# Performance work log

Hardware: AMD Instinct MI355X
Metric: run time of the kernel (lower is better)

Reference implementation:

```python
import jax, jax.numpy as jnp
import numpy as np

N, D, NUM_CLASSES = 4096, 512, 128
MARGIN = 0.3


def setup_inputs() -> dict:
    key = jax.random.key(0)
    k1, k2 = jax.random.split(key)
    embeddings = jax.random.normal(k1, (N, D), dtype=jnp.float32)
    labels = jax.random.randint(k2, (N,), 0, NUM_CLASSES, dtype=jnp.int64)
    return {"embeddings": embeddings, "labels": labels}


def _batch_hard_triplet(embeddings, labels, margin):
    # L2-normalize rows (torch F.normalize: x / max(||x||, eps))
    norm = jnp.linalg.norm(embeddings, axis=1, keepdims=True)
    e = embeddings / jnp.maximum(norm, 1e-12)
    n = e.shape[0]
    # Pairwise Euclidean distance via Gram matrix; ||a-b||^2 = 2 - 2 a.b for unit vectors
    gram = e @ e.T                                   # [N, N]
    sq = jnp.clip(2.0 - 2.0 * gram, 0.0, None)
    # safe sqrt: zero (and exactly-equal) pairs get distance 0 with zero gradient
    nz = sq > 0
    dist = jnp.where(nz, jnp.sqrt(jnp.where(nz, sq, 1.0)), 0.0)  # [N, N]

    same = labels[:, None] == labels[None, :]        # [N, N] bool
    eye = jnp.eye(n, dtype=bool)
    pos_mask = same & ~eye                           # positives excluding self
    neg_mask = ~same

    # hardest positive (row max over positives), hardest negative (row min over negatives)
    dist_ap = jnp.max(jnp.where(pos_mask, dist, -jnp.inf), axis=1)  # [N]
    dist_an = jnp.min(jnp.where(neg_mask, dist, jnp.inf), axis=1)   # [N]

    valid = jnp.any(pos_mask, axis=1) & jnp.any(neg_mask, axis=1)   # rows kept by torch loop
    per_row = jax.nn.relu(dist_ap - dist_an + margin)
    num_valid = jnp.sum(valid)
    loss_sum = jnp.sum(jnp.where(valid, per_row, 0.0))
    return jnp.where(num_valid > 0, loss_sum / jnp.maximum(num_valid, 1), 0.0)


def reference(embeddings, labels):
    return _batch_hard_triplet(embeddings, labels, MARGIN)
```

## Files before the change

### kernel.cpp

```cpp
#include <hip/hip_runtime.h>
#include <hip/hip_bf16.h>
#include <stdint.h>


#define NROW 4096
#define DIM  512
#define MARGIN 0.3f
#define BT 128
#define NTILE (NROW / BT)
#define NPAIR (NTILE * (NTILE + 1) / 2)
#define NBLK  (NPAIR * 2)
#define POS_INIT 0xFFFFFFFFu
#define NEG_INIT 0u

typedef __attribute__((ext_vector_type(8))) __bf16 bf16x8;
typedef __attribute__((ext_vector_type(4))) float  f32x4;
typedef __attribute__((ext_vector_type(8))) unsigned short u16x8;

__device__ __forceinline__ unsigned enc(float f) {
    unsigned u = __float_as_uint(f);
    return (u & 0x80000000u) ? ~u : (u | 0x80000000u);
}
__device__ __forceinline__ float dec(unsigned e) {
    return (e & 0x80000000u) ? __uint_as_float(e & 0x7fffffffu)
                             : __uint_as_float(~e);
}

__device__ __forceinline__ unsigned short f2bf(float f) {
    __hip_bfloat16 h = __float2bfloat16(f);
    return *reinterpret_cast<unsigned short*>(&h);
}

__global__ void tl_norm(const float* __restrict__ E,
                        __hip_bfloat16* __restrict__ Ebf,
                        unsigned* __restrict__ posArr,
                        unsigned* __restrict__ negArr) {
    if (blockIdx.x < 16) {
        int t = blockIdx.x * 256 + threadIdx.x;
        posArr[t] = POS_INIT;
        negArr[t] = NEG_INIT;
    }
    const int wave  = threadIdx.x >> 6;
    const int lane  = threadIdx.x & 63;
    const int r2    = lane >> 4;
    const int kc    = lane & 15;
    const int rtile = blockIdx.x;
    const int r_in  = wave * 4 + r2;
    const int row   = rtile * 16 + r_in;

    const float4* src = (const float4*)(E + (size_t)row * DIM) + kc * 8;
    float4 v[8];
    #pragma unroll
    for (int i = 0; i < 8; i++) v[i] = src[i];

    float ss = 0.0f;
    #pragma unroll
    for (int i = 0; i < 8; i++)
        ss += v[i].x*v[i].x + v[i].y*v[i].y + v[i].z*v[i].z + v[i].w*v[i].w;
    #pragma unroll
    for (int m = 1; m < 16; m <<= 1) ss += __shfl_xor(ss, m);
    const float inv = 1.0f / fmaxf(sqrtf(ss), 1e-12f);

    u16x8* dst = (u16x8*)Ebf + (size_t)kc * 16384 + (size_t)rtile * 64 + r_in;
    #pragma unroll
    for (int c = 0; c < 4; c++) {
        const float4 lo = v[2*c], hi = v[2*c + 1];
        u16x8 o;
        o[0] = f2bf(lo.x * inv); o[1] = f2bf(lo.y * inv);
        o[2] = f2bf(lo.z * inv); o[3] = f2bf(lo.w * inv);
        o[4] = f2bf(hi.x * inv); o[5] = f2bf(hi.y * inv);
        o[6] = f2bf(hi.z * inv); o[7] = f2bf(hi.w * inv);
        dst[c * 16] = o;
    }
}

__global__ void __launch_bounds__(256, 3)
tl_gram(const __hip_bfloat16* __restrict__ Ebf,
        const int* __restrict__ labels,
        unsigned* __restrict__ posArr,
        unsigned* __restrict__ negArr) {
    __shared__ int rowLab[BT];
    __shared__ int colLab[64];

    const int bid = blockIdx.x;
    const int swz = (bid & 7) * (NBLK / 8) + (bid >> 3);
    int t = swz >> 1;
    const int h = swz & 1;

    int bi = 0, rowlen = NTILE;
    while (t >= rowlen) { t -= rowlen; rowlen--; bi++; }
    const int bj = bi + t;

    const int tid  = threadIdx.x;
    const int wave = tid >> 6;
    const int lane = tid & 63;
    const int quad = lane >> 4;
    const int l16  = lane & 15;
    const int wr   = wave >> 1;
    const int wc   = wave & 1;
    const int tileI = bi * BT;
    const int tileJ = bj * BT + h * 64;
    const bool diag = (bi == bj);

    if (tid < BT)            rowLab[tid] = labels[tileI + tid];
    else if (tid < BT + 64)  colLab[tid - BT] = labels[tileJ + (tid - BT)];
    __syncthreads();

    const bf16x8* Ev = (const bf16x8*)Ebf;
    const bf16x8* Ea = Ev + ((tileI + wr * 64) >> 4) * 64 + lane;
    const bf16x8* Eb = Ev + ((tileJ + wc * 32) >> 4) * 64 + lane;

    f32x4 acc[4][2] = {};
    bf16x8 a[4][4], b[4][2];

    #pragma unroll
    for (int p = 0; p < 3; ++p) {
        #pragma unroll
        for (int mi = 0; mi < 4; mi++) a[p][mi] = Ea[p * 16384 + mi * 64];
        #pragma unroll
        for (int ni = 0; ni < 2; ni++) b[p][ni] = Eb[p * 16384 + ni * 64];
    }
    #pragma unroll
    for (int kk = 0; kk < 16; ++kk) {
        const int cur = kk & 3;
        if (kk + 3 < 16) {
            const int nx = (kk + 3) & 3;
            #pragma unroll
            for (int mi = 0; mi < 4; mi++)
                a[nx][mi] = Ea[(kk + 3) * 16384 + mi * 64];
            #pragma unroll
            for (int ni = 0; ni < 2; ni++)
                b[nx][ni] = Eb[(kk + 3) * 16384 + ni * 64];
        }
        #pragma unroll
        for (int mi = 0; mi < 4; mi++)
            #pragma unroll
            for (int ni = 0; ni < 2; ni++)
                acc[mi][ni] = __builtin_amdgcn_mfma_f32_16x16x32_bf16(
                    a[cur][mi], b[cur][ni], acc[mi][ni], 0, 0, 0);
    }

    int rl[16], cl[2], clocv[2];
    #pragma unroll
    for (int mi = 0; mi < 4; mi++)
        #pragma unroll
        for (int reg = 0; reg < 4; reg++)
            rl[mi * 4 + reg] = rowLab[wr * 64 + mi * 16 + quad * 4 + reg];
    #pragma unroll
    for (int ni = 0; ni < 2; ni++) {
        clocv[ni] = wc * 32 + ni * 16 + l16;
        cl[ni] = colLab[clocv[ni]];
    }

    #pragma unroll
    for (int mi = 0; mi < 4; mi++) {
        #pragma unroll
        for (int reg = 0; reg < 4; reg++) {
            const int rloc = wr * 64 + mi * 16 + quad * 4 + reg;
            const int lr   = rl[mi * 4 + reg];
            const int gi   = tileI + rloc;
            float pmin =  INFINITY;
            float nmax = -INFINITY;
            #pragma unroll
            for (int ni = 0; ni < 2; ni++) {
                const int gj  = tileJ + clocv[ni];
                const float g = acc[mi][ni][reg];
                const bool same = (lr == cl[ni]);
                if (same && gi != gj) pmin = fminf(pmin, g);
                if (!same)            nmax = fmaxf(nmax, g);
            }
            #pragma unroll
            for (int m = 1; m < 16; m <<= 1) {
                pmin = fminf(pmin, __shfl_xor(pmin, m));
                nmax = fmaxf(nmax, __shfl_xor(nmax, m));
            }
            if (l16 == 0) {
                if (pmin <  INFINITY) atomicMin(&posArr[gi], enc(pmin));
                if (nmax > -INFINITY) atomicMax(&negArr[gi], enc(nmax));
            }
        }
    }

    if (!diag) {
        #pragma unroll
        for (int ni = 0; ni < 2; ni++) {
            const int lc = cl[ni];
            const int gj = tileJ + clocv[ni];
            float pmin =  INFINITY;
            float nmax = -INFINITY;
            #pragma unroll
            for (int mi = 0; mi < 4; mi++) {
                #pragma unroll
                for (int reg = 0; reg < 4; reg++) {
                    const float g = acc[mi][ni][reg];
                    const bool same = (rl[mi * 4 + reg] == lc);
                    if (same) pmin = fminf(pmin, g);
                    else      nmax = fmaxf(nmax, g);
                }
            }
            pmin = fminf(pmin, __shfl_xor(pmin, 16));
            pmin = fminf(pmin, __shfl_xor(pmin, 32));
            nmax = fmaxf(nmax, __shfl_xor(nmax, 16));
            nmax = fmaxf(nmax, __shfl_xor(nmax, 32));
            if (quad == 0) {
                if (pmin <  INFINITY) atomicMin(&posArr[gj], enc(pmin));
                if (nmax > -INFINITY) atomicMax(&negArr[gj], enc(nmax));
            }
        }
    }
}

__global__ void tl_final(const unsigned* __restrict__ posArr,
                         const unsigned* __restrict__ negArr,
                         float* __restrict__ out) {
    const int tid = threadIdx.x;
    uint4 pe4 = ((const uint4*)posArr)[tid];
    uint4 ne4 = ((const uint4*)negArr)[tid];
    unsigned pes[4] = {pe4.x, pe4.y, pe4.z, pe4.w};
    unsigned nes[4] = {ne4.x, ne4.y, ne4.z, ne4.w};
    float sum = 0.0f;
    int   count = 0;
    #pragma unroll
    for (int j = 0; j < 4; j++) {
        const bool valid = (pes[j] != POS_INIT) && (nes[j] != NEG_INIT);
        const float dap = sqrtf(fmaxf(2.0f - 2.0f * dec(pes[j]), 0.0f));
        const float dan = sqrtf(fmaxf(2.0f - 2.0f * dec(nes[j]), 0.0f));
        const float per = fmaxf(dap - dan + MARGIN, 0.0f);
        if (valid) { sum += per; count += 1; }
    }
    #pragma unroll
    for (int m = 32; m >= 1; m >>= 1) {
        sum   += __shfl_xor(sum, m);
        count += __shfl_xor(count, m);
    }
    __shared__ float ssum[16];
    __shared__ int   scnt[16];
    const int wave = tid >> 6, lane = tid & 63;
    if (lane == 0) { ssum[wave] = sum; scnt[wave] = count; }
    __syncthreads();
    if (tid == 0) {
        float s = 0.0f; int c = 0;
        #pragma unroll
        for (int w = 0; w < 16; w++) { s += ssum[w]; c += scnt[w]; }
        out[0] = (c > 0) ? (s / (float)c) : 0.0f;
    }
}

extern "C" void kernel_launch(void* const* d_in, const int* in_sizes, int n_in,
                              void* d_out, int out_size, void* d_ws, size_t ws_size,
                              hipStream_t stream) {
    const float* E      = (const float*)d_in[0];
    const int*   labels = (const int*)d_in[1];
    float*       out    = (float*)d_out;

    char* ws = (char*)d_ws;
    __hip_bfloat16* Ebf   = (__hip_bfloat16*)ws;
    unsigned* posArr      = (unsigned*)(ws + (size_t)NROW * DIM * 2);
    unsigned* negArr      = posArr + NROW;

    tl_norm<<<NROW / 16, 256, 0, stream>>>(E, Ebf, posArr, negArr);
    tl_gram<<<NBLK, 256, 0, stream>>>(Ebf, labels, posArr, negArr);
    tl_final<<<1, 1024, 0, stream>>>(posArr, negArr, out);
}
```

Before: 101.9 us.

## Use full 128x128 Gram tiles per block instead of split 128x64 halves

Each block now computes a full 128x128 tile pair, so each wave computes a 64x64 sub-tile with 4x4 MFMA accumulators instead of 64x32. This halves the block count and raises operand reuse per loaded fragment, cutting global/L2 loads of B operands and duplicate row-side atomics. Occupancy drops (launch bounds 3→2) because register pressure increases, and sched_barriers are added to pin load/MFMA ordering. Only 528 blocks remain for 256 CUs, so wave quantization and load imbalance may get worse.

Result: faster. 92.60 us (-9.1%).

```diff
diff --git a/kernel.cpp b/kernel.cpp
--- a/kernel.cpp
+++ b/kernel.cpp
@@ -9,7 +9,6 @@
 #define BT 128
 #define NTILE (NROW / BT)
 #define NPAIR (NTILE * (NTILE + 1) / 2)
-#define NBLK  (NPAIR * 2)
 #define POS_INIT 0xFFFFFFFFu
 #define NEG_INIT 0u
 
@@ -74,18 +73,16 @@
     }
 }
 
-__global__ void __launch_bounds__(256, 3)
+__global__ void __launch_bounds__(256, 2)
 tl_gram(const __hip_bfloat16* __restrict__ Ebf,
         const int* __restrict__ labels,
         unsigned* __restrict__ posArr,
         unsigned* __restrict__ negArr) {
     __shared__ int rowLab[BT];
-    __shared__ int colLab[64];
+    __shared__ int colLab[BT];
 
     const int bid = blockIdx.x;
-    const int swz = (bid & 7) * (NBLK / 8) + (bid >> 3);
-    int t = swz >> 1;
-    const int h = swz & 1;
+    int t = (bid & 7) * (NPAIR / 8) + (bid >> 3);
 
     int bi = 0, rowlen = NTILE;
     while (t >= rowlen) { t -= rowlen; rowlen--; bi++; }
@@ -99,56 +96,60 @@
     const int wr   = wave >> 1;
     const int wc   = wave & 1;
     const int tileI = bi * BT;
-    const int tileJ = bj * BT + h * 64;
+    const int tileJ = bj * BT;
     const bool diag = (bi == bj);
 
-    if (tid < BT)            rowLab[tid] = labels[tileI + tid];
-    else if (tid < BT + 64)  colLab[tid - BT] = labels[tileJ + (tid - BT)];
+    if (tid < BT) rowLab[tid] = labels[tileI + tid];
+    else          colLab[tid - BT] = labels[tileJ + (tid - BT)];
     __syncthreads();
 
     const bf16x8* Ev = (const bf16x8*)Ebf;
     const bf16x8* Ea = Ev + ((tileI + wr * 64) >> 4) * 64 + lane;
-    const bf16x8* Eb = Ev + ((tileJ + wc * 32) >> 4) * 64 + lane;
-
-    f32x4 acc[4][2] = {};
-    bf16x8 a[4][4], b[4][2];
+    const bf16x8* Eb = Ev + ((tileJ + wc * 64) >> 4) * 64 + lane;
+
+    f32x4 acc[4][4] = {};
+    bf16x8 a[4][4], b[4][4];
 
     #pragma unroll
     for (int p = 0; p < 3; ++p) {
         #pragma unroll
-        for (int mi = 0; mi < 4; mi++) a[p][mi] = Ea[p * 16384 + mi * 64];
-        #pragma unroll
-        for (int ni = 0; ni < 2; ni++) b[p][ni] = Eb[p * 16384 + ni * 64];
-    }
+        for (int i = 0; i < 4; i++) {
+            a[p][i] = Ea[p * 16384 + i * 64];
+            b[p][i] = Eb[p * 16384 + i * 64];
+        }
+    }
+    __builtin_amdgcn_sched_barrier(0);
+
     #pragma unroll
     for (int kk = 0; kk < 16; ++kk) {
         const int cur = kk & 3;
         if (kk + 3 < 16) {
             const int nx = (kk + 3) & 3;
             #pragma unroll
-            for (int mi = 0; mi < 4; mi++)
-                a[nx][mi] = Ea[(kk + 3) * 16384 + mi * 64];
-            #pragma unroll
-            for (int ni = 0; ni < 2; ni++)
-                b[nx][ni] = Eb[(kk + 3) * 16384 + ni * 64];
-        }
+            for (int i = 0; i < 4; i++) {
+                a[nx][i] = Ea[(kk + 3) * 16384 + i * 64];
+                b[nx][i] = Eb[(kk + 3) * 16384 + i * 64];
+            }
+        }
+        __builtin_amdgcn_sched_barrier(0);
         #pragma unroll
         for (int mi = 0; mi < 4; mi++)
             #pragma unroll
-            for (int ni = 0; ni < 2; ni++)
+            for (int ni = 0; ni < 4; ni++)
                 acc[mi][ni] = __builtin_amdgcn_mfma_f32_16x16x32_bf16(
                     a[cur][mi], b[cur][ni], acc[mi][ni], 0, 0, 0);
-    }
-
-    int rl[16], cl[2], clocv[2];
+        __builtin_amdgcn_sched_barrier(0);
+    }
+
+    int rl[16], cl[4], clocv[4];
     #pragma unroll
     for (int mi = 0; mi < 4; mi++)
         #pragma unroll
         for (int reg = 0; reg < 4; reg++)
             rl[mi * 4 + reg] = rowLab[wr * 64 + mi * 16 + quad * 4 + reg];
     #pragma unroll
-    for (int ni = 0; ni < 2; ni++) {
-        clocv[ni] = wc * 32 + ni * 16 + l16;
+    for (int ni = 0; ni < 4; ni++) {
+        clocv[ni] = wc * 64 + ni * 16 + l16;
         cl[ni] = colLab[clocv[ni]];
     }
 
@@ -162,7 +163,7 @@
             float pmin =  INFINITY;
             float nmax = -INFINITY;
             #pragma unroll
-            for (int ni = 0; ni < 2; ni++) {
+            for (int ni = 0; ni < 4; ni++) {
                 const int gj  = tileJ + clocv[ni];
                 const float g = acc[mi][ni][reg];
                 const bool same = (lr == cl[ni]);
@@ -183,7 +184,7 @@
 
     if (!diag) {
         #pragma unroll
-        for (int ni = 0; ni < 2; ni++) {
+        for (int ni = 0; ni < 4; ni++) {
             const int lc = cl[ni];
             const int gj = tileJ + clocv[ni];
             float pmin =  INFINITY;
@@ -259,6 +260,6 @@
     unsigned* negArr      = posArr + NROW;
 
     tl_norm<<<NROW / 16, 256, 0, stream>>>(E, Ebf, posArr, negArr);
-    tl_gram<<<NBLK, 256, 0, stream>>>(Ebf, labels, posArr, negArr);
+    tl_gram<<<NPAIR, 256, 0, stream>>>(Ebf, labels, posArr, negArr);
     tl_final<<<1, 1024, 0, stream>>>(posArr, negArr, out);
 }
```
